# Performance work log

Hardware: AMD Instinct MI355X
Metric: run time of the kernel (lower is better)

Reference implementation:

```python
import jax, jax.numpy as jnp
import numpy as np

N = 32768      # nodes
E = 524288     # edges (avg degree 16)
F = 64         # node_feat_dim
D = 64         # gnn_dim (= per-head out channels, concat=False)
ED = 32        # edge_feat_dim
L = 6          # num_layers
H = 2          # heads
C = D          # per-head channels
LN_EPS = 1e-5


def layer_norm(h, g, b):
    mu = jnp.mean(h, axis=-1, keepdims=True)
    var = jnp.mean((h - mu) ** 2, axis=-1, keepdims=True)
    return g * (h - mu) * jax.lax.rsqrt(var + LN_EPS) + b


def setup_inputs() -> dict:
    key = jax.random.key(0)
    ks = jax.random.split(key, 16)
    x = jax.random.normal(ks[0], (N, F), jnp.float32)
    edge_index = jax.random.randint(ks[1], (2, E), 0, N, jnp.int32)
    edge_attr = jax.random.normal(ks[2], (E, ED), jnp.float32)
    manual_gamma = 1.0 + 0.1 * jax.random.normal(ks[3], (L, D), jnp.float32)
    manual_beta = 0.1 * jax.random.normal(ks[4], (L, D), jnp.float32)
    # node_embed Linear(F, D)
    embed_W = jax.random.normal(ks[5], (F, D), jnp.float32) / np.float32(np.sqrt(F))
    embed_b = jnp.zeros((D,), jnp.float32)
    # per-layer LayerNorm affine params
    ln_gamma = jnp.ones((L, D), jnp.float32)
    ln_beta = jnp.zeros((L, D), jnp.float32)
    # per-layer GATConv params (shared lin for src/dst, PyG non-bipartite)
    lin_W = jax.random.normal(ks[6], (L, D, H * C), jnp.float32) / np.float32(np.sqrt(D))
    lin_edge_W = jax.random.normal(ks[7], (L, ED, H * C), jnp.float32) / np.float32(np.sqrt(ED))
    att_src = jax.random.normal(ks[8], (L, H, C), jnp.float32) / np.float32(np.sqrt(C))
    att_dst = jax.random.normal(ks[9], (L, H, C), jnp.float32) / np.float32(np.sqrt(C))
    att_edge = jax.random.normal(ks[10], (L, H, C), jnp.float32) / np.float32(np.sqrt(C))
    gat_bias = jnp.zeros((L, C), jnp.float32)
    # edge output head: Linear(2D+ED, D) -> ReLU -> Linear(D, 1)
    head_W1 = jax.random.normal(ks[11], (2 * D + ED, D), jnp.float32) / np.float32(np.sqrt(2 * D + ED))
    head_b1 = jnp.zeros((D,), jnp.float32)
    head_W2 = jax.random.normal(ks[12], (D, 1), jnp.float32) / np.float32(np.sqrt(D))
    head_b2 = jnp.zeros((1,), jnp.float32)
    return dict(x=x, edge_index=edge_index, edge_attr=edge_attr,
                manual_gamma=manual_gamma, manual_beta=manual_beta,
                embed_W=embed_W, embed_b=embed_b, ln_gamma=ln_gamma, ln_beta=ln_beta,
                lin_W=lin_W, lin_edge_W=lin_edge_W, att_src=att_src, att_dst=att_dst,
                att_edge=att_edge, gat_bias=gat_bias, head_W1=head_W1, head_b1=head_b1,
                head_W2=head_W2, head_b2=head_b2)


def reference(x, edge_index, edge_attr, manual_gamma, manual_beta,
              embed_W, embed_b, ln_gamma, ln_beta, lin_W, lin_edge_W,
              att_src, att_dst, att_edge, gat_bias, head_W1, head_b1,
              head_W2, head_b2):
    src, dst = edge_index[0], edge_index[1]
    # PyG GATConv default add_self_loops=True, fill_value='mean' for edge_attr
    loop = jnp.arange(N, dtype=edge_index.dtype)
    src_f = jnp.concatenate([src, loop])   # [E+N]
    dst_f = jnp.concatenate([dst, loop])
    deg = jax.ops.segment_sum(jnp.ones((E,), x.dtype), dst, num_segments=N)
    loop_attr = jax.ops.segment_sum(edge_attr, dst, num_segments=N) / jnp.maximum(deg, 1.0)[:, None]
    edge_attr_f = jnp.concatenate([edge_attr, loop_attr], axis=0)  # [E+N, ED]

    h = x @ embed_W + embed_b  # [N, D]
    for l in range(L):
        hn = layer_norm(h, ln_gamma[l], ln_beta[l])
        hm = manual_gamma[l][None, :] * hn + manual_beta[l][None, :]
        xh = (hm @ lin_W[l]).reshape(N, H, C)                      # [N,H,C]
        a_s = jnp.sum(xh * att_src[l][None], axis=-1)              # [N,H]
        a_d = jnp.sum(xh * att_dst[l][None], axis=-1)              # [N,H]
        eh = (edge_attr_f @ lin_edge_W[l]).reshape(-1, H, C)       # [E+N,H,C]
        a_e = jnp.sum(eh * att_edge[l][None], axis=-1)             # [E+N,H]
        alpha = jax.nn.leaky_relu(a_s[src_f] + a_d[dst_f] + a_e, 0.2)
        amax = jax.ops.segment_max(alpha, dst_f, num_segments=N)   # every node has a self-loop
        ex = jnp.exp(alpha - amax[dst_f])
        den = jax.ops.segment_sum(ex, dst_f, num_segments=N)
        w = ex / (den[dst_f] + 1e-16)                              # segment softmax [E+N,H]
        msg = xh[src_f] * w[..., None]                             # [E+N,H,C]
        out = jax.ops.segment_sum(msg, dst_f, num_segments=N)      # [N,H,C]
        h = jax.nn.relu(jnp.mean(out, axis=1) + gat_bias[l])       # concat=False -> head mean

    ef = jnp.concatenate([h[src], h[dst], edge_attr], axis=-1)     # [E, 2D+ED]
    hid = jax.nn.relu(ef @ head_W1 + head_b1)
    return (hid @ head_W2 + head_b2)[:, 0]                         # [E]
```

## Files before the change

### kernel.cpp

```cpp
#include <hip/hip_runtime.h>
#include <hip/hip_bf16.h>
#include <math.h>

#define NN 32768
#define EE 524288
#define LL 6

typedef __attribute__((ext_vector_type(8))) short short8;
typedef __attribute__((ext_vector_type(4))) float floatx4;
typedef __attribute__((ext_vector_type(4))) float fx4;

union U16x8 { short8 v; unsigned short u[8]; };

__device__ __forceinline__ unsigned short f2bf(float x) {
    union { float f; unsigned int u; } v; v.f = x;
    unsigned int r = v.u + 0x7fffu + ((v.u >> 16) & 1u);
    return (unsigned short)(r >> 16);
}
__device__ __forceinline__ float bf2f(unsigned short h) {
    union { unsigned int u; float f; } v; v.u = (unsigned int)h << 16;
    return v.f;
}


__global__ void deg_kernel(const int* __restrict__ dst, int* __restrict__ deg) {
    int i = (blockIdx.x * 256 + threadIdx.x) * 4;
    int4 d = *(const int4*)(dst + i);
    atomicAdd(&deg[d.x], 1);
    atomicAdd(&deg[d.y], 1);
    atomicAdd(&deg[d.z], 1);
    atomicAdd(&deg[d.w], 1);
}

__global__ __launch_bounds__(1024) void scan_kernel(const int* __restrict__ deg,
                                                    int* __restrict__ row_ptr,
                                                    int* __restrict__ cnt) {
    __shared__ int bs[1024];
    int t = threadIdx.x;
    int base = t * 32;
    int loc[32];
    int s = 0;
#pragma unroll
    for (int i = 0; i < 32; ++i) { int v = deg[base + i]; loc[i] = s; s += v; }
    bs[t] = s;
    __syncthreads();
    for (int off = 1; off < 1024; off <<= 1) {
        int v = (t >= off) ? bs[t - off] : 0;
        __syncthreads();
        bs[t] += v;
        __syncthreads();
    }
    int pre = (t == 0) ? 0 : bs[t - 1];
#pragma unroll
    for (int i = 0; i < 32; ++i) { row_ptr[base + i] = pre + loc[i]; cnt[base + i] = 0; }
    if (t == 1023) row_ptr[NN] = bs[1023];
}

__global__ void fill_kernel(const int* __restrict__ src, const int* __restrict__ dst,
                            const int* __restrict__ row_ptr, int* __restrict__ cnt,
                            int2* __restrict__ sedge) {
    int e = blockIdx.x * 256 + threadIdx.x;
    if (e >= EE) return;
    int d = dst[e];
    int pos = row_ptr[d] + atomicAdd(&cnt[d], 1);
    sedge[pos] = make_int2(e, src[e]);
}

__global__ __launch_bounds__(256) void smallprep_kernel(
    const float* __restrict__ lin_W, const float* __restrict__ head_W1,
    const float* __restrict__ lin_edge_W, const float* __restrict__ att_edge,
    const float* __restrict__ att_src, const float* __restrict__ att_dst,
    unsigned short* __restrict__ gBhi, unsigned short* __restrict__ gBlo,
    unsigned short* __restrict__ aeBhi, unsigned short* __restrict__ aeBlo,
    float* __restrict__ vs, float* __restrict__ vvd,
    unsigned short* __restrict__ w1chi, unsigned short* __restrict__ w1clo,
    int* __restrict__ deg) {
    __shared__ float svb[384];
    int bb = blockIdx.x;
    int tid = threadIdx.x;
    if (bb < 7) {
        unsigned short* dh = gBhi + (size_t)bb * 128 * 64;
        unsigned short* dl = gBlo + (size_t)bb * 128 * 64;
        if (bb < 6) {
            int n2 = tid & 63, kh = tid >> 6;
            U16x8 hh[4], ll[4];
            for (int kk = 0; kk < 32; ++kk) {
                int j = kh * 32 + kk;
                int h = j >> 6, k = j & 63;
                float wv = 0.5f * lin_W[((size_t)bb * 64 + k) * 128 + h * 64 + n2];
                unsigned short h16 = f2bf(wv);
                hh[kk >> 3].u[kk & 7] = h16;
                ll[kk >> 3].u[kk & 7] = f2bf(wv - bf2f(h16));
            }
#pragma unroll
            for (int c = 0; c < 4; ++c) {
                int cg = kh * 4 + c;
                int off = n2 * 128 + ((cg ^ (n2 & 15)) << 3);
                *(short8*)(dh + off) = hh[c].v;
                *(short8*)(dl + off) = ll[c].v;
            }
        } else {
            int n = tid & 127, kh = tid >> 7;
            U16x8 hh[4], ll[4];
            for (int kk = 0; kk < 32; ++kk) {
                int k = kh * 32 + kk;
                float wv = (n < 64) ? head_W1[k * 64 + n] : head_W1[(64 + k) * 64 + (n - 64)];
                unsigned short h16 = f2bf(wv);
                hh[kk >> 3].u[kk & 7] = h16;
                ll[kk >> 3].u[kk & 7] = f2bf(wv - bf2f(h16));
            }
#pragma unroll
            for (int c = 0; c < 4; ++c) {
                int cg = kh * 4 + c;
                int off = n * 64 + ((cg ^ (n & 7)) << 3);
                *(short8*)(dh + off) = hh[c].v;
                *(short8*)(dl + off) = ll[c].v;
            }
        }
    } else if (bb == 7) {
        for (int t = tid; t < 384; t += 256) {
            int l = t / 64; int r = t & 63; int ed = r >> 1; int hh = r & 1;
            const float* w = lin_edge_W + l * 32 * 128 + ed * 128 + hh * 64;
            const float* a = att_edge + l * 128 + hh * 64;
            float s = 0.f;
#pragma unroll 8
            for (int c = 0; c < 64; ++c) s += w[c] * a[c];
            svb[t] = s;
        }
        int n = tid & 63, kc = tid >> 6;
#pragma unroll
        for (int j = 0; j < 8; ++j) {
            int k = kc * 8 + j;
            float wv = head_W1[(128 + k) * 64 + n];
            unsigned short h16 = f2bf(wv);
            w1chi[n * 32 + k] = h16;
            w1clo[n * 32 + k] = f2bf(wv - bf2f(h16));
        }
        __syncthreads();
        if (tid < 64) {
            int n2 = tid & 15, q = tid >> 4;
            U16x8 hi, lo;
#pragma unroll
            for (int i = 0; i < 8; ++i) {
                int k = q * 8 + i;
                float val = (n2 < 12) ? svb[(n2 >> 1) * 64 + k * 2 + (n2 & 1)] : 0.f;
                unsigned short h16 = f2bf(val);
                hi.u[i] = h16;
                lo.u[i] = f2bf(val - bf2f(h16));
            }
            *(short8*)(aeBhi + tid * 8) = hi.v;
            *(short8*)(aeBlo + tid * 8) = lo.v;
        }
    } else if (bb < 14) {
        int l = bb - 8;
        int sel = tid >> 7, idx = tid & 127;
        int h = idx >> 6, k = idx & 63;
        const float* att = (sel ? att_dst : att_src) + l * 128 + h * 64;
        const float* wr = lin_W + ((size_t)l * 64 + k) * 128 + h * 64;
        float s = 0.f;
#pragma unroll 8
        for (int c = 0; c < 64; ++c) s += wr[c] * att[c];
        (sel ? vvd : vs)[l * 128 + idx] = s;
    } else {
        int i = (bb - 14) * 1024 + tid * 4;
        *(int4*)(deg + i) = make_int4(0, 0, 0, 0);
    }
}

__global__ __launch_bounds__(256) void ae_csr_kernel(
    const float* __restrict__ edge_attr, const int2* __restrict__ sedge,
    const unsigned short* __restrict__ aeBhi, const unsigned short* __restrict__ aeBlo,
    float* __restrict__ aeL) {
    __shared__ float tr[4][64 * 13];
    int tid = threadIdx.x;
    int w = tid >> 6, lane = tid & 63;
    int p0 = blockIdx.x * 256 + w * 64;
    short8 bhi = *(const short8*)(aeBhi + lane * 8);
    short8 blo = *(const short8*)(aeBlo + lane * 8);
    int r = lane & 15, q = lane >> 4;
    float* trw = tr[w];
#pragma unroll
    for (int t = 0; t < 4; ++t) {
        int eg = sedge[p0 + t * 16 + r].x;
        const fx4* p = (const fx4*)(edge_attr + (size_t)eg * 32 + q * 8);
        fx4 f0 = p[0], f1 = p[1];
        float av[8] = {f0.x, f0.y, f0.z, f0.w, f1.x, f1.y, f1.z, f1.w};
        U16x8 hi, lo;
#pragma unroll
        for (int jj = 0; jj < 8; ++jj) {
            unsigned short h16 = f2bf(av[jj]);
            hi.u[jj] = h16;
            lo.u[jj] = f2bf(av[jj] - bf2f(h16));
        }
        floatx4 acc = {};
        acc = __builtin_amdgcn_mfma_f32_16x16x32_bf16(lo.v, bhi, acc, 0, 0, 0);
        acc = __builtin_amdgcn_mfma_f32_16x16x32_bf16(hi.v, blo, acc, 0, 0, 0);
        acc = __builtin_amdgcn_mfma_f32_16x16x32_bf16(hi.v, bhi, acc, 0, 0, 0);
        if (r < 12) {
#pragma unroll
            for (int rr = 0; rr < 4; ++rr)
                trw[(t * 16 + q * 4 + rr) * 13 + r] = acc[rr];
        }
    }
    int2 sl = sedge[p0 + lane];
#pragma unroll
    for (int l = 0; l < LL; ++l) {
        fx4 rec;
        rec.x = __int_as_float(sl.y);
        rec.y = trw[lane * 13 + l * 2];
        rec.z = trw[lane * 13 + l * 2 + 1];
        rec.w = 0.f;
        __builtin_nontemporal_store(rec, (fx4*)(aeL + ((size_t)l * EE + p0 + lane) * 4));
    }
}

__global__ __launch_bounds__(256) void embed_ln_kernel(
    const float* __restrict__ x, const float* __restrict__ W, const float* __restrict__ b,
    const float* __restrict__ ln_g, const float* __restrict__ ln_b,
    const float* __restrict__ mg, const float* __restrict__ mb,
    const float* __restrict__ vs0, const float* __restrict__ vd0,
    unsigned short* __restrict__ hm_bf, float* __restrict__ a_s, float* __restrict__ a_d) {
    __shared__ float xr[4][64];
    int w = threadIdx.x >> 6, j = threadIdx.x & 63;
    int n = blockIdx.x * 4 + w;
    xr[w][j] = x[(size_t)n * 64 + j];
    __syncthreads();
    float acc = b[j];
#pragma unroll 8
    for (int k = 0; k < 64; ++k) acc += xr[w][k] * W[k * 64 + j];
    float s = acc, sq = acc * acc;
    for (int off = 1; off < 64; off <<= 1) { s += __shfl_xor(s, off); sq += __shfl_xor(sq, off); }
    float mu = s * (1.f / 64.f);
    float var = sq * (1.f / 64.f) - mu * mu;
    float rs = rsqrtf(var + 1e-5f);
    float hm = mg[j] * (ln_g[j] * (acc - mu) * rs + ln_b[j]) + mb[j];
    hm_bf[(size_t)n * 64 + j] = f2bf(hm);
    float s0 = hm * vs0[j], s1 = hm * vs0[64 + j];
    float d0 = hm * vd0[j], d1 = hm * vd0[64 + j];
    for (int off = 1; off < 64; off <<= 1) {
        s0 += __shfl_xor(s0, off); s1 += __shfl_xor(s1, off);
        d0 += __shfl_xor(d0, off); d1 += __shfl_xor(d1, off);
    }
    if (j == 0) {
        a_s[n * 2] = s0; a_s[n * 2 + 1] = s1;
        a_d[n * 2] = d0; a_d[n * 2 + 1] = d1;
    }
}

__device__ __forceinline__ void fma8h(uint4 pv, float w, float* a) {
    unsigned int u[4] = {pv.x, pv.y, pv.z, pv.w};
#pragma unroll
    for (int q = 0; q < 4; ++q) {
        union { unsigned int x; float f; } lo, hi;
        lo.x = u[q] << 16; hi.x = u[q] & 0xffff0000u;
        a[2 * q]     += w * lo.f;
        a[2 * q + 1] += w * hi.f;
    }
}

__device__ __forceinline__ void agg_node(
    int n, int ch, int hh, int j, const uint4* hmv, const float2* as2,
    const float* ad_in, const float* aeLl, const int* row_ptr, float* sg, U16x8& hb) {
    float2 adn = ((const float2*)ad_in)[n];
    float2 asn = as2[n];
    uint4 pvself = hmv[(size_t)n * 8 + ch];
    int beg = row_ptr[n], end = row_ptr[n + 1];
    int degn = end - beg;
    float acc[8] = {};
    float den = 0.f, aex = 0.f, aey = 0.f;
    for (int base = 0; base < degn; base += 64) {
        int cnt = degn - base; cnt = cnt > 64 ? 64 : cnt;
        int nchunk = (cnt + 15) >> 4;
        for (int it = 0; it < nchunk; ++it) {
            int s0 = it * 16;
            int rem = cnt - s0;
            float w0v = 0.f, w1v = 0.f;
            int sval = 0;
            if (j < rem) {
                fx4 rv = *(const fx4*)(aeLl + ((size_t)(beg + base + s0 + j)) * 4);
                int sv = __float_as_int(rv.x);
                float2 as = as2[sv];
                aex += rv.y; aey += rv.z;
                float al0 = as.x + adn.x + rv.y; al0 = al0 > 0.f ? al0 : 0.2f * al0;
                float al1 = as.y + adn.y + rv.z; al1 = al1 > 0.f ? al1 : 0.2f * al1;
                w0v = __expf(al0);
                w1v = __expf(al1);
                sval = sv;
            }
            float4 st;
            st.x = __int_as_float(sval); st.y = w0v; st.z = w1v; st.w = 0.f;
            *(float4*)(sg + (s0 + j) * 4) = st;
        }
        int c8 = (cnt + 7) & ~7;
        for (int s = 0; s < c8; s += 8) {
            float4 m[8];
#pragma unroll
            for (int u = 0; u < 8; ++u) m[u] = *(const float4*)(sg + (s + u) * 4);
            uint4 p[8];
#pragma unroll
            for (int u = 0; u < 8; ++u) p[u] = hmv[(size_t)__float_as_int(m[u].x) * 8 + ch];
#pragma unroll
            for (int u = 0; u < 8; ++u) {
                float b = hh ? m[u].z : m[u].y;
                den += b;
                fma8h(p[u], b, acc);
            }
        }
    }
#pragma unroll
    for (int m = 1; m < 16; m <<= 1) {
        aex += __shfl_xor(aex, m);
        aey += __shfl_xor(aey, m);
    }
    float invd = 1.f / fmaxf((float)degn, 1.f);
    float al0 = asn.x + adn.x + aex * invd; al0 = al0 > 0.f ? al0 : 0.2f * al0;
    float al1 = asn.y + adn.y + aey * invd; al1 = al1 > 0.f ? al1 : 0.2f * al1;
    float ws = hh ? __expf(al1) : __expf(al0);
    den += ws;
    fma8h(pvself, ws, acc);
    float inv = 1.f / (den + 1e-16f);
#pragma unroll
    for (int q = 0; q < 8; ++q) hb.u[q] = f2bf(acc[q] * inv);
}

__global__ __launch_bounds__(256) void fused_post(
    const unsigned short* __restrict__ hm_in, const float* __restrict__ as_in,
    const float* __restrict__ ad_in, const float* __restrict__ aeLl,
    const int* __restrict__ row_ptr,
    const unsigned short* __restrict__ gBhi, const unsigned short* __restrict__ gBlo,
    const float* __restrict__ bias, const float* __restrict__ ln_g,
    const float* __restrict__ ln_b, const float* __restrict__ mg,
    const float* __restrict__ mb, const float* __restrict__ vsn,
    const float* __restrict__ vdn, unsigned short* __restrict__ hm_out,
    float* __restrict__ as_out, float* __restrict__ ad_out) {
    __shared__ char smem[49152];
    unsigned short* Ahi = (unsigned short*)smem;
    float* stgAll = (float*)(smem + 16384);
    unsigned short* Bhi = (unsigned short*)(smem + 16384);
    unsigned short* Blo = (unsigned short*)(smem + 32768);
    int tid = threadIdx.x;
    int w = tid >> 6, lane = tid & 63;
    int g = lane >> 4, j = lane & 15;
    int ch = j & 7, hh = j >> 3;
    const float2* as2 = (const float2*)as_in;
    const uint4* hmv = (const uint4*)hm_in;
    float* sg = stgAll + w * 1024 + g * 256;
    int nb = blockIdx.x * 64;

    for (int rr = 0; rr < 4; ++rr) {
        int m = w * 16 + rr * 4 + g;
        U16x8 hb;
        agg_node(nb + m, ch, hh, j, hmv, as2, ad_in, aeLl, row_ptr, sg, hb);
        int cg = hh * 8 + ch;
        *(short8*)(Ahi + m * 128 + ((cg ^ (m & 15)) << 3)) = hb.v;
    }
    __syncthreads();
    {
        const uint4* sh = (const uint4*)gBhi;
        const uint4* sl = (const uint4*)gBlo;
        for (int i = tid; i < 1024; i += 256) {
            ((uint4*)Bhi)[i] = sh[i];
            ((uint4*)Blo)[i] = sl[i];
        }
    }
    __syncthreads();

    int col = lane & 15, quad = lane >> 4;
    int m = w * 16 + col;
    floatx4 acc[4] = {};
#pragma unroll
    for (int s = 0; s < 4; ++s) {
        int ca = (quad + 4 * s) ^ col;
        short8 ahi = *(const short8*)(Ahi + m * 128 + ca * 8);
#pragma unroll
        for (int t = 0; t < 4; ++t) {
            int off = (t * 16 + col) * 128 + ca * 8;
            short8 bhi = *(const short8*)(Bhi + off);
            short8 blo = *(const short8*)(Blo + off);
            acc[t] = __builtin_amdgcn_mfma_f32_16x16x32_bf16(ahi, blo, acc[t], 0, 0, 0);
            acc[t] = __builtin_amdgcn_mfma_f32_16x16x32_bf16(ahi, bhi, acc[t], 0, 0, 0);
        }
    }
    int nodebase = nb + w * 16;
    float bv[4];
#pragma unroll
    for (int t = 0; t < 4; ++t) bv[t] = bias[t * 16 + col];
    float vsv[4], vsv1[4], vdv[4], vdv1[4], lg[4], lb[4], mgv[4], mbv[4];
#pragma unroll
    for (int t = 0; t < 4; ++t) {
        int c = t * 16 + col;
        vsv[t] = vsn[c]; vsv1[t] = vsn[64 + c];
        vdv[t] = vdn[c]; vdv1[t] = vdn[64 + c];
        lg[t] = ln_g[c]; lb[t] = ln_b[c];
        mgv[t] = mg[c]; mbv[t] = mb[c];
    }
#pragma unroll
    for (int r = 0; r < 4; ++r) {
        int node = nodebase + quad * 4 + r;
        float hv[4];
        float s = 0.f, sq = 0.f;
#pragma unroll
        for (int t = 0; t < 4; ++t) {
            float v = acc[t][r] + bv[t];
            v = v > 0.f ? v : 0.f;
            hv[t] = v;
            s += v; sq += v * v;
        }
        for (int off = 1; off < 16; off <<= 1) { s += __shfl_xor(s, off); sq += __shfl_xor(sq, off); }
        float mu = s * (1.f / 64.f);
        float var = sq * (1.f / 64.f) - mu * mu;
        float rs = rsqrtf(var + 1e-5f);
        float s0 = 0.f, s1 = 0.f, d0 = 0.f, d1 = 0.f;
#pragma unroll
        for (int t = 0; t < 4; ++t) {
            float hmval = mgv[t] * (lg[t] * (hv[t] - mu) * rs + lb[t]) + mbv[t];
            hm_out[(size_t)node * 64 + t * 16 + col] = f2bf(hmval);
            s0 += hmval * vsv[t]; s1 += hmval * vsv1[t];
            d0 += hmval * vdv[t]; d1 += hmval * vdv1[t];
        }
        for (int off = 1; off < 16; off <<= 1) {
            s0 += __shfl_xor(s0, off); s1 += __shfl_xor(s1, off);
            d0 += __shfl_xor(d0, off); d1 += __shfl_xor(d1, off);
        }
        if (col == 0) {
            as_out[node * 2] = s0; as_out[node * 2 + 1] = s1;
            ad_out[node * 2] = d0; ad_out[node * 2 + 1] = d1;
        }
    }
}

__global__ __launch_bounds__(256) void fused_uv(
    const unsigned short* __restrict__ hm_in, const float* __restrict__ as_in,
    const float* __restrict__ ad_in, const float* __restrict__ aeLl,
    const int* __restrict__ row_ptr,
    const unsigned short* __restrict__ gB5hi, const unsigned short* __restrict__ gB5lo,
    const float* __restrict__ bias,
    const unsigned short* __restrict__ gB6hi, const unsigned short* __restrict__ gB6lo,
    unsigned short* __restrict__ uv) {
    __shared__ char smem[49152];
    unsigned short* Ahi  = (unsigned short*)smem;
    float* stgAll        = (float*)(smem + 16384);
    unsigned short* B5hi = (unsigned short*)(smem + 16384);
    unsigned short* B5lo = (unsigned short*)(smem + 32768);
    unsigned short* A2hi = (unsigned short*)smem;
    unsigned short* A2lo = (unsigned short*)(smem + 8192);
    unsigned short* B6hi = (unsigned short*)(smem + 16384);
    unsigned short* B6lo = (unsigned short*)(smem + 32768);
    int tid = threadIdx.x;
    int w = tid >> 6, lane = tid & 63;
    int g = lane >> 4, j = lane & 15;
    int ch = j & 7, hh = j >> 3;
    const float2* as2 = (const float2*)as_in;
    const uint4* hmv = (const uint4*)hm_in;
    float* sg = stgAll + w * 1024 + g * 256;
    int nb = blockIdx.x * 64;

    for (int rr = 0; rr < 4; ++rr) {
        int m = w * 16 + rr * 4 + g;
        U16x8 hb;
        agg_node(nb + m, ch, hh, j, hmv, as2, ad_in, aeLl, row_ptr, sg, hb);
        int cg = hh * 8 + ch;
        *(short8*)(Ahi + m * 128 + ((cg ^ (m & 15)) << 3)) = hb.v;
    }
    __syncthreads();
    {
        const uint4* sh = (const uint4*)gB5hi;
        const uint4* sl = (const uint4*)gB5lo;
        for (int i = tid; i < 1024; i += 256) {
            ((uint4*)B5hi)[i] = sh[i];
            ((uint4*)B5lo)[i] = sl[i];
        }
    }
    __syncthreads();

    int col = lane & 15, quad = lane >> 4;
    int m = w * 16 + col;
    floatx4 acc[4] = {};
#pragma unroll
    for (int s = 0; s < 4; ++s) {
        int ca = (quad + 4 * s) ^ col;
        short8 ahi = *(const short8*)(Ahi + m * 128 + ca * 8);
#pragma unroll
        for (int t = 0; t < 4; ++t) {
            int off = (t * 16 + col) * 128 + ca * 8;
            short8 bhi = *(const short8*)(B5hi + off);
            short8 blo = *(const short8*)(B5lo + off);
            acc[t] = __builtin_amdgcn_mfma_f32_16x16x32_bf16(ahi, blo, acc[t], 0, 0, 0);
            acc[t] = __builtin_amdgcn_mfma_f32_16x16x32_bf16(ahi, bhi, acc[t], 0, 0, 0);
        }
    }
    float bv[4];
#pragma unroll
    for (int t = 0; t < 4; ++t) bv[t] = bias[t * 16 + col];
    __syncthreads();
#pragma unroll
    for (int t = 0; t < 4; ++t) {
        int c = t * 16 + col;
        int cg = c >> 3, cr = c & 7;
#pragma unroll
        for (int r = 0; r < 4; ++r) {
            float v = acc[t][r] + bv[t];
            v = v > 0.f ? v : 0.f;
            int i = w * 16 + quad * 4 + r;
            int off = i * 64 + ((cg ^ (i & 7)) << 3) + cr;
            unsigned short hhv = f2bf(v);
            A2hi[off] = hhv;
            A2lo[off] = f2bf(v - bf2f(hhv));
        }
    }
    for (int i = tid; i < 1024; i += 256) {
        ((uint4*)B6hi)[i] = ((const uint4*)gB6hi)[i];
        ((uint4*)B6lo)[i] = ((const uint4*)gB6lo)[i];
    }
    __syncthreads();

    floatx4 acc2[8] = {};
#pragma unroll
    for (int s = 0; s < 2; ++s) {
        int ca = (quad + 4 * s) ^ (col & 7);
        short8 a2h = *(const short8*)(A2hi + m * 64 + ca * 8);
        short8 a2l = *(const short8*)(A2lo + m * 64 + ca * 8);
#pragma unroll
        for (int t = 0; t < 8; ++t) {
            int off = (t * 16 + col) * 64 + ca * 8;
            short8 bh = *(const short8*)(B6hi + off);
            short8 bl = *(const short8*)(B6lo + off);
            acc2[t] = __builtin_amdgcn_mfma_f32_16x16x32_bf16(a2l, bh, acc2[t], 0, 0, 0);
            acc2[t] = __builtin_amdgcn_mfma_f32_16x16x32_bf16(a2h, bl, acc2[t], 0, 0, 0);
            acc2[t] = __builtin_amdgcn_mfma_f32_16x16x32_bf16(a2h, bh, acc2[t], 0, 0, 0);
        }
    }
    int nodebase = nb + w * 16;
#pragma unroll
    for (int t = 0; t < 8; ++t)
#pragma unroll
        for (int r = 0; r < 4; ++r)
            uv[(size_t)(nodebase + quad * 4 + r) * 128 + t * 16 + col] = f2bf(acc2[t][r]);
}

__global__ __launch_bounds__(256) void head2_kernel(
    const unsigned short* __restrict__ uv, const int* __restrict__ src,
    const int* __restrict__ dst, const float* __restrict__ edge_attr,
    const unsigned short* __restrict__ w1chi, const unsigned short* __restrict__ w1clo,
    const float* __restrict__ b1, const float* __restrict__ W2,
    const float* __restrict__ b2, float* __restrict__ out) {
    __shared__ float g[64][68];
    __shared__ unsigned short Abf[64 * 40];
    __shared__ unsigned short Bh[64 * 40], Bl[64 * 40];
    __shared__ int sA[64], dA[64];
    int tid = threadIdx.x;
    int base = blockIdx.x * 64;
    if (tid < 64) sA[tid] = src[base + tid];
    else if (tid < 128) dA[tid - 64] = dst[base + tid - 64];
    {
        int n = tid >> 2, c = tid & 3;
        *(short8*)(Bh + n * 40 + c * 8) = *(const short8*)(w1chi + n * 32 + c * 8);
        *(short8*)(Bl + n * 40 + c * 8) = *(const short8*)(w1clo + n * 32 + c * 8);
    }
    {
        int e = tid >> 2, q = tid & 3;
        const fx4* p = (const fx4*)(edge_attr + (size_t)(base + e) * 32 + q * 8);
        fx4 f0 = __builtin_nontemporal_load(p);
        fx4 f1 = __builtin_nontemporal_load(p + 1);
        float av[8] = {f0.x, f0.y, f0.z, f0.w, f1.x, f1.y, f1.z, f1.w};
        U16x8 cv;
#pragma unroll
        for (int jj = 0; jj < 8; ++jj) cv.u[jj] = f2bf(av[jj]);
        *(short8*)(Abf + e * 40 + q * 8) = cv.v;
    }
    __syncthreads();
    {
        int e = tid >> 2, q = tid & 3;
        const uint4* su = (const uint4*)(uv + (size_t)sA[e] * 128);
        const uint4* dv = (const uint4*)(uv + (size_t)dA[e] * 128);
        uint4 U0 = su[2 * q], U1 = su[2 * q + 1];
        uint4 V0 = dv[8 + 2 * q], V1 = dv[9 + 2 * q];
        const float4* b1p = (const float4*)(b1 + q * 16);
        float bb[16];
#pragma unroll
        for (int jj = 0; jj < 4; ++jj) {
            float4 b4 = b1p[jj];
            bb[4 * jj] = b4.x; bb[4 * jj + 1] = b4.y; bb[4 * jj + 2] = b4.z; bb[4 * jj + 3] = b4.w;
        }
        unsigned int uw[8] = {U0.x, U0.y, U0.z, U0.w, U1.x, U1.y, U1.z, U1.w};
        unsigned int vw[8] = {V0.x, V0.y, V0.z, V0.w, V1.x, V1.y, V1.z, V1.w};
        float* gr = &g[e][q * 16];
#pragma unroll
        for (int jj = 0; jj < 8; ++jj) {
            gr[2 * jj] = bf2f((unsigned short)(uw[jj] & 0xffff)) +
                         bf2f((unsigned short)(vw[jj] & 0xffff)) + bb[2 * jj];
            gr[2 * jj + 1] = bf2f((unsigned short)(uw[jj] >> 16)) +
                             bf2f((unsigned short)(vw[jj] >> 16)) + bb[2 * jj + 1];
        }
    }
    __syncthreads();

    int lane = tid & 63, w = tid >> 6, col = lane & 15, quad = lane >> 4;
    short8 a = *(const short8*)(Abf + (w * 16 + col) * 40 + quad * 8);
    floatx4 acc[4] = {};
#pragma unroll
    for (int t = 0; t < 4; ++t) {
        int off = (t * 16 + col) * 40 + quad * 8;
        short8 bh = *(const short8*)(Bh + off);
        short8 bl = *(const short8*)(Bl + off);
        acc[t] = __builtin_amdgcn_mfma_f32_16x16x32_bf16(a, bl, acc[t], 0, 0, 0);
        acc[t] = __builtin_amdgcn_mfma_f32_16x16x32_bf16(a, bh, acc[t], 0, 0, 0);
    }
    float sv[4] = {0.f, 0.f, 0.f, 0.f};
#pragma unroll
    for (int t = 0; t < 4; ++t) {
        float w2v = W2[t * 16 + col];
#pragma unroll
        for (int r = 0; r < 4; ++r) {
            float hid = acc[t][r] + g[w * 16 + quad * 4 + r][t * 16 + col];
            hid = hid > 0.f ? hid : 0.f;
            sv[r] += hid * w2v;
        }
    }
    float b2v = b2[0];
#pragma unroll
    for (int r = 0; r < 4; ++r) {
        float v = sv[r];
        v += __shfl_xor(v, 1);
        v += __shfl_xor(v, 2);
        v += __shfl_xor(v, 4);
        v += __shfl_xor(v, 8);
        if (col == 0) out[base + w * 16 + quad * 4 + r] = v + b2v;
    }
}


extern "C" void kernel_launch(void* const* d_in, const int* in_sizes, int n_in,
                              void* d_out, int out_size, void* d_ws, size_t ws_size,
                              hipStream_t stream) {
    const float* x            = (const float*)d_in[0];
    const int*   edge_index   = (const int*)d_in[1];
    const float* edge_attr    = (const float*)d_in[2];
    const float* manual_gamma = (const float*)d_in[3];
    const float* manual_beta  = (const float*)d_in[4];
    const float* embed_W      = (const float*)d_in[5];
    const float* embed_b      = (const float*)d_in[6];
    const float* ln_gamma     = (const float*)d_in[7];
    const float* ln_beta      = (const float*)d_in[8];
    const float* lin_W        = (const float*)d_in[9];
    const float* lin_edge_W   = (const float*)d_in[10];
    const float* att_src      = (const float*)d_in[11];
    const float* att_dst      = (const float*)d_in[12];
    const float* att_edge     = (const float*)d_in[13];
    const float* gat_bias     = (const float*)d_in[14];
    const float* head_W1      = (const float*)d_in[15];
    const float* head_b1      = (const float*)d_in[16];
    const float* head_W2      = (const float*)d_in[17];
    const float* head_b2      = (const float*)d_in[18];
    float* out = (float*)d_out;

    const int* src = edge_index;
    const int* dst = edge_index + EE;

    char* ws = (char*)d_ws;
    size_t off = 0;
    auto alloc = [&](size_t bytes) {
        void* p = ws + off;
        off += (bytes + 255) & ~(size_t)255;
        return p;
    };
    int*   deg        = (int*)alloc(NN * 4);
    int*   row_ptr    = (int*)alloc((NN + 1) * 4);
    int*   cnt        = (int*)alloc(NN * 4);
    int2*  sedge      = (int2*)alloc((size_t)EE * 8);
    float* aeL        = (float*)alloc((size_t)LL * EE * 16);
    float* vs         = (float*)alloc(LL * 128 * 4);
    float* vvd        = (float*)alloc(LL * 128 * 4);
    float* asA        = (float*)alloc((size_t)NN * 2 * 4);
    float* asB        = (float*)alloc((size_t)NN * 2 * 4);
    float* adA        = (float*)alloc((size_t)NN * 2 * 4);
    float* adB        = (float*)alloc((size_t)NN * 2 * 4);
    unsigned short* hmA   = (unsigned short*)alloc((size_t)NN * 64 * 2);
    unsigned short* hmB   = (unsigned short*)alloc((size_t)NN * 64 * 2);
    unsigned short* uvbuf = (unsigned short*)alloc((size_t)NN * 128 * 2);
    unsigned short* gBhi  = (unsigned short*)alloc((size_t)7 * 128 * 64 * 2);
    unsigned short* gBlo  = (unsigned short*)alloc((size_t)7 * 128 * 64 * 2);
    unsigned short* w1chi = (unsigned short*)alloc(64 * 32 * 2);
    unsigned short* w1clo = (unsigned short*)alloc(64 * 32 * 2);
    unsigned short* aeBhi = (unsigned short*)alloc(64 * 8 * 2);
    unsigned short* aeBlo = (unsigned short*)alloc(64 * 8 * 2);
    if (off > ws_size) return;

    smallprep_kernel<<<46, 256, 0, stream>>>(lin_W, head_W1, lin_edge_W, att_edge,
                                             att_src, att_dst, gBhi, gBlo, aeBhi, aeBlo,
                                             vs, vvd, w1chi, w1clo, deg);
    deg_kernel<<<EE / 1024, 256, 0, stream>>>(dst, deg);
    scan_kernel<<<1, 1024, 0, stream>>>(deg, row_ptr, cnt);
    fill_kernel<<<EE / 256, 256, 0, stream>>>(src, dst, row_ptr, cnt, sedge);
    ae_csr_kernel<<<EE / 256, 256, 0, stream>>>(edge_attr, sedge, aeBhi, aeBlo, aeL);
    embed_ln_kernel<<<NN / 4, 256, 0, stream>>>(x, embed_W, embed_b, ln_gamma, ln_beta,
                                                manual_gamma, manual_beta, vs, vvd,
                                                hmA, asA, adA);

    for (int l = 0; l < LL; ++l) {
        const unsigned short* hin = (l & 1) ? hmB : hmA;
        unsigned short* hout = (l & 1) ? hmA : hmB;
        const float* asi = (l & 1) ? asB : asA;
        float* aso = (l & 1) ? asA : asB;
        const float* adi = (l & 1) ? adB : adA;
        float* ado = (l & 1) ? adA : adB;
        const float* aeLl = aeL + (size_t)l * EE * 4;
        if (l < LL - 1) {
            fused_post<<<NN / 64, 256, 0, stream>>>(
                hin, asi, adi, aeLl, row_ptr,
                gBhi + (size_t)l * 128 * 64, gBlo + (size_t)l * 128 * 64,
                gat_bias + l * 64, ln_gamma + (l + 1) * 64, ln_beta + (l + 1) * 64,
                manual_gamma + (l + 1) * 64, manual_beta + (l + 1) * 64,
                vs + (l + 1) * 128, vvd + (l + 1) * 128, hout, aso, ado);
        } else {
            fused_uv<<<NN / 64, 256, 0, stream>>>(
                hin, asi, adi, aeLl, row_ptr,
                gBhi + (size_t)l * 128 * 64, gBlo + (size_t)l * 128 * 64,
                gat_bias + l * 64, gBhi + (size_t)6 * 128 * 64,
                gBlo + (size_t)6 * 128 * 64, uvbuf);
        }
    }

    head2_kernel<<<EE / 64, 256, 0, stream>>>(uvbuf, src, dst, edge_attr, w1chi, w1clo,
                                              head_b1, head_W2, head_b2, out);
}
```

Measured before the change: 444.1 us.

## Batch edge-score gathers for four nodes per group before aggregation

Replaces the per-node aggregation routine with a batched version. It first issues the row_ptr, edge-record and source-score gathers for the first 32 edges of all four nodes a 16-lane group handles, computes their softmax weights and stages them in shared memory, then runs the feature gathers node by node. Edges beyond 32 use the old chunked loop. The aim is more memory-level parallelism on the dependent gather chains, which were serialised per node before; the cost is more registers and twice the shared staging space per warp.

```diff
diff --git a/kernel.cpp b/kernel.cpp
--- a/kernel.cpp
+++ b/kernel.cpp
@@ -258,69 +258,136 @@
     }
 }
 
-__device__ __forceinline__ void agg_node(
-    int n, int ch, int hh, int j, const uint4* hmv, const float2* as2,
-    const float* ad_in, const float* aeLl, const int* row_ptr, float* sg, U16x8& hb) {
-    float2 adn = ((const float2*)ad_in)[n];
-    float2 asn = as2[n];
-    uint4 pvself = hmv[(size_t)n * 8 + ch];
-    int beg = row_ptr[n], end = row_ptr[n + 1];
-    int degn = end - beg;
-    float acc[8] = {};
-    float den = 0.f, aex = 0.f, aey = 0.f;
-    for (int base = 0; base < degn; base += 64) {
-        int cnt = degn - base; cnt = cnt > 64 ? 64 : cnt;
-        int nchunk = (cnt + 15) >> 4;
-        for (int it = 0; it < nchunk; ++it) {
-            int s0 = it * 16;
-            int rem = cnt - s0;
-            float w0v = 0.f, w1v = 0.f;
-            int sval = 0;
-            if (j < rem) {
-                fx4 rv = *(const fx4*)(aeLl + ((size_t)(beg + base + s0 + j)) * 4);
-                int sv = __float_as_int(rv.x);
-                float2 as = as2[sv];
-                aex += rv.y; aey += rv.z;
-                float al0 = as.x + adn.x + rv.y; al0 = al0 > 0.f ? al0 : 0.2f * al0;
-                float al1 = as.y + adn.y + rv.z; al1 = al1 > 0.f ? al1 : 0.2f * al1;
-                w0v = __expf(al0);
-                w1v = __expf(al1);
-                sval = sv;
-            }
-            float4 st;
-            st.x = __int_as_float(sval); st.y = w0v; st.z = w1v; st.w = 0.f;
-            *(float4*)(sg + (s0 + j) * 4) = st;
-        }
-        int c8 = (cnt + 7) & ~7;
+__device__ __forceinline__ void agg_batch(
+    int nb, int w, int g, int j, int ch, int hh,
+    const uint4* hmv, const float2* as2, const float* ad_in,
+    const float* aeLl, const int* row_ptr, float* stgW, unsigned short* Ahi) {
+    int begA[4], degA[4];
+    float2 adn4[4], asn4[4];
+#pragma unroll
+    for (int rr = 0; rr < 4; ++rr) {
+        int n = nb + w * 16 + rr * 4 + g;
+        begA[rr] = row_ptr[n];
+        degA[rr] = row_ptr[n + 1] - begA[rr];
+        adn4[rr] = ((const float2*)ad_in)[n];
+        asn4[rr] = as2[n];
+    }
+    fx4 rv[8];
+#pragma unroll
+    for (int u = 0; u < 8; ++u) {
+        int rr = u >> 1, s = ((u & 1) << 4) + j;
+        if (s < degA[rr]) {
+            rv[u] = *(const fx4*)(aeLl + (size_t)(begA[rr] + s) * 4);
+        } else {
+            rv[u].x = 0.f; rv[u].y = 0.f; rv[u].z = 0.f; rv[u].w = 0.f;
+        }
+    }
+    float2 asv[8];
+#pragma unroll
+    for (int u = 0; u < 8; ++u) {
+        int rr = u >> 1, s = ((u & 1) << 4) + j;
+        asv[u] = (s < degA[rr]) ? as2[__float_as_int(rv[u].x)] : make_float2(0.f, 0.f);
+    }
+    float aexA[4] = {0.f, 0.f, 0.f, 0.f}, aeyA[4] = {0.f, 0.f, 0.f, 0.f};
+#pragma unroll
+    for (int u = 0; u < 8; ++u) {
+        int rr = u >> 1, s = ((u & 1) << 4) + j;
+        float w0v = 0.f, w1v = 0.f;
+        int sval = 0;
+        if (s < degA[rr]) {
+            aexA[rr] += rv[u].y; aeyA[rr] += rv[u].z;
+            float al0 = asv[u].x + adn4[rr].x + rv[u].y; al0 = al0 > 0.f ? al0 : 0.2f * al0;
+            float al1 = asv[u].y + adn4[rr].y + rv[u].z; al1 = al1 > 0.f ? al1 : 0.2f * al1;
+            w0v = __expf(al0);
+            w1v = __expf(al1);
+            sval = __float_as_int(rv[u].x);
+        }
+        float4 st;
+        st.x = __int_as_float(sval); st.y = w0v; st.z = w1v; st.w = 0.f;
+        *(float4*)(stgW + ((rr * 4 + g) << 7) + s * 4) = st;
+    }
+#pragma unroll 1
+    for (int rr = 0; rr < 4; ++rr) {
+        float* sg = stgW + ((rr * 4 + g) << 7);
+        int n = nb + w * 16 + rr * 4 + g;
+        int degn = degA[rr];
+        uint4 pvself = hmv[(size_t)n * 8 + ch];
+        float acc[8] = {};
+        float den = 0.f;
+        float aex = aexA[rr], aey = aeyA[rr];
+        int cnt0 = degn > 32 ? 32 : degn;
+        int c8 = (cnt0 + 7) & ~7;
         for (int s = 0; s < c8; s += 8) {
-            float4 m[8];
-#pragma unroll
-            for (int u = 0; u < 8; ++u) m[u] = *(const float4*)(sg + (s + u) * 4);
+            float4 m4[8];
+#pragma unroll
+            for (int u = 0; u < 8; ++u) m4[u] = *(const float4*)(sg + (s + u) * 4);
             uint4 p[8];
 #pragma unroll
-            for (int u = 0; u < 8; ++u) p[u] = hmv[(size_t)__float_as_int(m[u].x) * 8 + ch];
+            for (int u = 0; u < 8; ++u) p[u] = hmv[(size_t)__float_as_int(m4[u].x) * 8 + ch];
 #pragma unroll
             for (int u = 0; u < 8; ++u) {
-                float b = hh ? m[u].z : m[u].y;
+                float b = hh ? m4[u].z : m4[u].y;
                 den += b;
                 fma8h(p[u], b, acc);
             }
         }
-    }
-#pragma unroll
-    for (int m = 1; m < 16; m <<= 1) {
-        aex += __shfl_xor(aex, m);
-        aey += __shfl_xor(aey, m);
-    }
-    float invd = 1.f / fmaxf((float)degn, 1.f);
-    float al0 = asn.x + adn.x + aex * invd; al0 = al0 > 0.f ? al0 : 0.2f * al0;
-    float al1 = asn.y + adn.y + aey * invd; al1 = al1 > 0.f ? al1 : 0.2f * al1;
-    float ws = hh ? __expf(al1) : __expf(al0);
-    den += ws;
-    fma8h(pvself, ws, acc);
-    float inv = 1.f / (den + 1e-16f);
-#pragma unroll
-    for (int q = 0; q < 8; ++q) hb.u[q] = f2bf(acc[q] * inv);
+        for (int base = 32; base < degn; base += 32) {
+            int cnt = degn - base; cnt = cnt > 32 ? 32 : cnt;
+            int nchunk = (cnt + 15) >> 4;
+            for (int it = 0; it < nchunk; ++it) {
+                int s0 = it * 16;
+                int rem = cnt - s0;
+                float w0v = 0.f, w1v = 0.f;
+                int sval = 0;
+                if (j < rem) {
+                    fx4 rvx = *(const fx4*)(aeLl + (size_t)(begA[rr] + base + s0 + j) * 4);
+                    float2 asx = as2[__float_as_int(rvx.x)];
+                    aex += rvx.y; aey += rvx.z;
+                    float al0 = asx.x + adn4[rr].x + rvx.y; al0 = al0 > 0.f ? al0 : 0.2f * al0;
+                    float al1 = asx.y + adn4[rr].y + rvx.z; al1 = al1 > 0.f ? al1 : 0.2f * al1;
+                    w0v = __expf(al0);
+                    w1v = __expf(al1);
+                    sval = __float_as_int(rvx.x);
+                }
+                float4 st;
+                st.x = __int_as_float(sval); st.y = w0v; st.z = w1v; st.w = 0.f;
+                *(float4*)(sg + (s0 + j) * 4) = st;
+            }
+            int cc8 = (cnt + 7) & ~7;
+            for (int s = 0; s < cc8; s += 8) {
+                float4 m4[8];
+#pragma unroll
+                for (int u = 0; u < 8; ++u) m4[u] = *(const float4*)(sg + (s + u) * 4);
+                uint4 p[8];
+#pragma unroll
+                for (int u = 0; u < 8; ++u) p[u] = hmv[(size_t)__float_as_int(m4[u].x) * 8 + ch];
+#pragma unroll
+                for (int u = 0; u < 8; ++u) {
+                    float b = hh ? m4[u].z : m4[u].y;
+                    den += b;
+                    fma8h(p[u], b, acc);
+                }
+            }
+        }
+#pragma unroll
+        for (int m = 1; m < 16; m <<= 1) {
+            aex += __shfl_xor(aex, m);
+            aey += __shfl_xor(aey, m);
+        }
+        float invd = 1.f / fmaxf((float)degn, 1.f);
+        float al0 = asn4[rr].x + adn4[rr].x + aex * invd; al0 = al0 > 0.f ? al0 : 0.2f * al0;
+        float al1 = asn4[rr].y + adn4[rr].y + aey * invd; al1 = al1 > 0.f ? al1 : 0.2f * al1;
+        float ws = hh ? __expf(al1) : __expf(al0);
+        den += ws;
+        fma8h(pvself, ws, acc);
+        float inv = 1.f / (den + 1e-16f);
+        U16x8 hb;
+#pragma unroll
+        for (int q = 0; q < 8; ++q) hb.u[q] = f2bf(acc[q] * inv);
+        int m = w * 16 + rr * 4 + g;
+        int cg = hh * 8 + ch;
+        *(short8*)(Ahi + m * 128 + ((cg ^ (m & 15)) << 3)) = hb.v;
+    }
 }
 
 __global__ __launch_bounds__(256) void fused_post(
@@ -344,16 +411,10 @@
     int ch = j & 7, hh = j >> 3;
     const float2* as2 = (const float2*)as_in;
     const uint4* hmv = (const uint4*)hm_in;
-    float* sg = stgAll + w * 1024 + g * 256;
     int nb = blockIdx.x * 64;
 
-    for (int rr = 0; rr < 4; ++rr) {
-        int m = w * 16 + rr * 4 + g;
-        U16x8 hb;
-        agg_node(nb + m, ch, hh, j, hmv, as2, ad_in, aeLl, row_ptr, sg, hb);
-        int cg = hh * 8 + ch;
-        *(short8*)(Ahi + m * 128 + ((cg ^ (m & 15)) << 3)) = hb.v;
-    }
+    agg_batch(nb, w, g, j, ch, hh, hmv, as2, ad_in, aeLl, row_ptr,
+              stgAll + w * 2048, Ahi);
     __syncthreads();
     {
         const uint4* sh = (const uint4*)gBhi;
@@ -452,16 +513,10 @@
     int ch = j & 7, hh = j >> 3;
     const float2* as2 = (const float2*)as_in;
     const uint4* hmv = (const uint4*)hm_in;
-    float* sg = stgAll + w * 1024 + g * 256;
     int nb = blockIdx.x * 64;
 
-    for (int rr = 0; rr < 4; ++rr) {
-        int m = w * 16 + rr * 4 + g;
-        U16x8 hb;
-        agg_node(nb + m, ch, hh, j, hmv, as2, ad_in, aeLl, row_ptr, sg, hb);
-        int cg = hh * 8 + ch;
-        *(short8*)(Ahi + m * 128 + ((cg ^ (m & 15)) << 3)) = hb.v;
-    }
+    agg_batch(nb, w, g, j, ch, hh, hmv, as2, ad_in, aeLl, row_ptr,
+              stgAll + w * 2048, Ahi);
     __syncthreads();
     {
         const uint4* sh = (const uint4*)gB5hi;
```

After: 454.1 us. 1.02x slower.
